# Kernel tuning notes

Measured on AMD Instinct MI355X. Metric: run time of the kernel, lower is better.

## Reference

```python
import jax, jax.numpy as jnp
import numpy as np
from jax import lax

I, H, D1 = 130, 10, 20  # input_size, hidden_size, linear1 width


def _gru_last(x, Wih, Whh, bih, bhh):
    """PyTorch-convention GRU (gate order r,z,n); returns last hidden state [B,H]."""
    # Precompute input projections for all timesteps: [B,T,3H]
    xi = jnp.einsum('bti,gi->btg', x, Wih) + bih
    h0 = jnp.zeros((x.shape[0], H), x.dtype)

    def step(h, xt):  # xt: [B,3H]
        gh = h @ Whh.T + bhh  # [B,3H]
        r = jax.nn.sigmoid(xt[:, :H] + gh[:, :H])
        z = jax.nn.sigmoid(xt[:, H:2 * H] + gh[:, H:2 * H])
        n = jnp.tanh(xt[:, 2 * H:] + r * gh[:, 2 * H:])
        h_new = (1.0 - z) * n + z * h
        return h_new, None

    hT, _ = lax.scan(step, h0, jnp.swapaxes(xi, 0, 1))  # scan over time
    return hT


def setup_inputs() -> dict:
    key = jax.random.key(0)
    ks = jax.random.split(key, 12)
    B, T = 2048, 128
    s_ih = 1.0 / np.sqrt(H)
    inp = {
        'ru': jax.random.normal(ks[0], (B, T, I), jnp.float32),
        'en': jax.random.normal(ks[1], (B, T, I), jnp.float32),
        'ru_Wih': jax.random.uniform(ks[2], (3 * H, I), jnp.float32, -s_ih, s_ih),
        'ru_Whh': jax.random.uniform(ks[3], (3 * H, H), jnp.float32, -s_ih, s_ih),
        'ru_bih': jax.random.uniform(ks[4], (3 * H,), jnp.float32, -s_ih, s_ih),
        'ru_bhh': jax.random.uniform(ks[5], (3 * H,), jnp.float32, -s_ih, s_ih),
        'en_Wih': jax.random.uniform(ks[6], (3 * H, I), jnp.float32, -s_ih, s_ih),
        'en_Whh': jax.random.uniform(ks[7], (3 * H, H), jnp.float32, -s_ih, s_ih),
        'en_bih': jax.random.uniform(ks[8], (3 * H,), jnp.float32, -s_ih, s_ih),
        'en_bhh': jax.random.uniform(ks[9], (3 * H,), jnp.float32, -s_ih, s_ih),
        'W1': jax.random.uniform(ks[10], (D1, 2 * H), jnp.float32, -1 / np.sqrt(2 * H), 1 / np.sqrt(2 * H)),
        'b1': jnp.zeros((D1,), jnp.float32),
        'W2': jax.random.uniform(ks[11], (1, D1), jnp.float32, -1 / np.sqrt(D1), 1 / np.sqrt(D1)),
        'b2': jnp.zeros((1,), jnp.float32),
    }
    return inp


def reference(ru, en, ru_Wih, ru_Whh, ru_bih, ru_bhh,
              en_Wih, en_Whh, en_bih, en_bhh, W1, b1, W2, b2):
    ru_h = _gru_last(ru, ru_Wih, ru_Whh, ru_bih, ru_bhh)  # [B,H] (last timestep output)
    en_h = _gru_last(en, en_Wih, en_Whh, en_bih, en_bhh)  # [B,H]
    grus_out = jnp.concatenate([ru_h, en_h], axis=1)       # [B,2H]
    h1 = grus_out @ W1.T + b1                              # [B,20] (no activation in original)
    out = h1 @ W2.T + b2                                   # [B,1]
    return out
```

## Files before the change

kernel.cpp:

```cpp
#include <hip/hip_runtime.h>


#define BB 2048
#define TT 128
#define II 130

__device__ __forceinline__ float sigmoidf_fast(float x) {
    return __fdividef(1.f, 1.f + __expf(-x));
}
__device__ __forceinline__ float tanhf_fast(float x) {
    float ax = fabsf(x);
    float e = __expf(-2.f * ax);
    float t = __fdividef(1.f - e, 1.f + e);
    return copysignf(t, x);
}

__global__ __launch_bounds__(256, 4)
void gru_fused(const float* __restrict__ ru, const float* __restrict__ en,
               const float* __restrict__ ruWih, const float* __restrict__ ruWhh,
               const float* __restrict__ rubih, const float* __restrict__ rubhh,
               const float* __restrict__ enWih, const float* __restrict__ enWhh,
               const float* __restrict__ enbih, const float* __restrict__ enbhh,
               const float* __restrict__ W1, const float* __restrict__ b1,
               const float* __restrict__ W2, const float* __restrict__ b2,
               float* __restrict__ out)
{
    const int tid  = threadIdx.x;
    const int wv   = tid >> 6;
    const int lane = tid & 63;
    const int g    = lane & 31;
    const int h    = lane >> 5;
    const int wid  = blockIdx.x * 4 + wv;
    const int gru  = wid >> 11;
    const int b    = wid & (BB - 1);

    const float* __restrict__ x   = gru ? en    : ru;
    const float* __restrict__ Wih = gru ? enWih : ruWih;
    const float* __restrict__ Whh = gru ? enWhh : ruWhh;
    const float* __restrict__ bih = gru ? enbih : rubih;
    const float* __restrict__ bhh = gru ? enbhh : rubhh;

    __shared__ __align__(16) float lds[4][176];
    float* __restrict__ X    = lds[wv];
    float* __restrict__ PRE  = X + 132;
    float* __restrict__ Hbuf = X + 164;

    const int gq = (g < 30) ? g : 0;
    float wih[64];
    #pragma unroll
    for (int j = 0; j < 64; ++j) wih[j] = Wih[gq * II + h * 64 + j];
    const float w_e = Wih[gq * II + 128 + h];
    float whh[10];
    #pragma unroll
    for (int k = 0; k < 10; ++k) whh[k] = Whh[gq * 10 + k];
    const float bihg = bih[gq];
    const float bhhg = bhh[gq];

    if (lane < 12) Hbuf[lane] = 0.f;
    float hown = 0.f;

    const float* __restrict__ xrow = x + (size_t)b * (TT * II);

    float xa = xrow[lane];
    float xb = xrow[64 + lane];
    float xc = (lane < 2) ? xrow[128 + lane] : 0.f;

    for (int t = 0; t < TT; ++t) {
        X[lane] = xa;
        X[64 + lane] = xb;
        if (lane < 2) X[128 + lane] = xc;

        {
            const int tn = (t < TT - 1) ? t + 1 : t;
            const float* __restrict__ xn = xrow + (size_t)tn * II;
            xa = xn[lane];
            xb = xn[64 + lane];
            xc = (lane < 2) ? xn[128 + lane] : 0.f;
        }

        const float4 h03 = *(const float4*)(Hbuf);
        const float4 h47 = *(const float4*)(Hbuf + 4);
        const float2 h89 = *(const float2*)(Hbuf + 8);
        float gh0 = fmaf(whh[0], h03.x, bhhg);
        float gh1 = whh[1] * h03.y;
        gh0 = fmaf(whh[2], h03.z, gh0);
        gh1 = fmaf(whh[3], h03.w, gh1);
        gh0 = fmaf(whh[4], h47.x, gh0);
        gh1 = fmaf(whh[5], h47.y, gh1);
        gh0 = fmaf(whh[6], h47.z, gh0);
        gh1 = fmaf(whh[7], h47.w, gh1);
        gh0 = fmaf(whh[8], h89.x, gh0);
        gh1 = fmaf(whh[9], h89.y, gh1);
        const float gh = gh0 + gh1;

        float s0 = 0.f, s1 = 0.f, s2 = 0.f, s3 = 0.f;
        const float4* __restrict__ xb4 = (const float4*)(X + h * 64);
        #pragma unroll
        for (int c = 0; c < 16; ++c) {
            const float4 v = xb4[c];
            s0 = fmaf(wih[4 * c + 0], v.x, s0);
            s1 = fmaf(wih[4 * c + 1], v.y, s1);
            s2 = fmaf(wih[4 * c + 2], v.z, s2);
            s3 = fmaf(wih[4 * c + 3], v.w, s3);
        }
        float s = (s0 + s1) + (s2 + s3);
        s = fmaf(w_e, X[128 + h], s);
        s += __shfl_xor(s, 32);

        const float xi  = s + bihg;
        const float pre = xi + gh;

        if (lane < 30) PRE[lane] = pre;
        const float rpre = PRE[(g - 20) & 31];
        const float zpre = PRE[(g - 10) & 31];

        const float r = sigmoidf_fast(rpre);
        const float z = sigmoidf_fast(zpre);
        const float n = tanhf_fast(xi + r * gh);
        const float hnew = (1.f - z) * n + z * hown;
        hown = hnew;

        if (lane >= 20 && lane < 30) Hbuf[lane - 20] = hnew;
    }

    float val = 0.f;
    if (lane < 10) {
        const float hk = Hbuf[lane];
        float v = 0.f;
        #pragma unroll
        for (int d = 0; d < 20; ++d)
            v = fmaf(W2[d], W1[d * 20 + gru * 10 + lane], v);
        val = v * hk;
        if (lane == 0 && gru == 0) {
            float c = b2[0];
            #pragma unroll
            for (int d = 0; d < 20; ++d) c = fmaf(W2[d], b1[d], c);
            val += c;
        }
    }
    #pragma unroll
    for (int o = 32; o > 0; o >>= 1) val += __shfl_xor(val, o);
    if (lane == 0) atomicAdd(&out[b], val);
}

extern "C" void kernel_launch(void* const* d_in, const int* in_sizes, int n_in,
                              void* d_out, int out_size, void* d_ws, size_t ws_size,
                              hipStream_t stream) {
    (void)in_sizes; (void)n_in; (void)d_ws; (void)ws_size;
    const float* ru    = (const float*)d_in[0];
    const float* en    = (const float*)d_in[1];
    const float* ruWih = (const float*)d_in[2];
    const float* ruWhh = (const float*)d_in[3];
    const float* rubih = (const float*)d_in[4];
    const float* rubhh = (const float*)d_in[5];
    const float* enWih = (const float*)d_in[6];
    const float* enWhh = (const float*)d_in[7];
    const float* enbih = (const float*)d_in[8];
    const float* enbhh = (const float*)d_in[9];
    const float* W1    = (const float*)d_in[10];
    const float* b1    = (const float*)d_in[11];
    const float* W2    = (const float*)d_in[12];
    const float* b2    = (const float*)d_in[13];
    float* out = (float*)d_out;

    hipMemsetAsync(d_out, 0, (size_t)out_size * sizeof(float), stream);
    gru_fused<<<dim3(1024), dim3(256), 0, stream>>>(
        ru, en, ruWih, ruWhh, rubih, rubhh,
        enWih, enWhh, enbih, enbhh, W1, b1, W2, b2, out);
}
```

Before: 143.7 us.

## Split GRU into parallel input-projection GEMM and lightweight recurrent scan kernel

Precomputes input projections for all timesteps into a workspace buffer with a separate fully parallel kernel. A second kernel then runs the recurrence, packing two batch chains per wavefront with per-gate hidden weights in registers. This removes the large input dot product from the serial per-timestep critical path. The cost is extra global memory traffic to write and re-read the projections, and it falls back to the fused kernel if the workspace is too small.

```diff
diff --git a/kernel.cpp b/kernel.cpp
--- a/kernel.cpp
+++ b/kernel.cpp
@@ -4,6 +4,8 @@
 #define BB 2048
 #define TT 128
 #define II 130
+#define ROWS_PER_GRU (BB * TT)
+#define ROWS_TOTAL   (2 * ROWS_PER_GRU)
 
 __device__ __forceinline__ float sigmoidf_fast(float x) {
     return __fdividef(1.f, 1.f + __expf(-x));
@@ -13,6 +15,169 @@
     float e = __expf(-2.f * ax);
     float t = __fdividef(1.f - e, 1.f + e);
     return copysignf(t, x);
+}
+
+__global__ __launch_bounds__(256, 4)
+void xi_gemm(const float* __restrict__ ru, const float* __restrict__ en,
+             const float* __restrict__ ruWih, const float* __restrict__ rubih,
+             const float* __restrict__ enWih, const float* __restrict__ enbih,
+             float* __restrict__ xi)
+{
+    const int tid  = threadIdx.x;
+    const int wv   = tid >> 6;
+    const int lane = tid & 63;
+    const int g    = lane & 31;
+    const int h    = lane >> 5;
+    const int w    = blockIdx.x * 4 + wv;
+    const int gru  = (w >= 4096);
+    const long row0 = (long)w * 64;
+
+    const float* __restrict__ x   = gru ? en    : ru;
+    const float* __restrict__ Wih = gru ? enWih : ruWih;
+    const float* __restrict__ bih = gru ? enbih : rubih;
+
+    const int gq = (g < 30) ? g : 0;
+    float wih[64];
+    #pragma unroll
+    for (int j = 0; j < 64; ++j) wih[j] = Wih[gq * II + h * 64 + j];
+    const float w_e  = Wih[gq * II + 128 + h];
+    const float bihg = bih[gq];
+
+    __shared__ __align__(16) float lds[4][132];
+    float* __restrict__ X = lds[wv];
+
+    const long r0l = row0 - (long)gru * ROWS_PER_GRU;
+    const float* __restrict__ xrow = x + r0l * II;
+    float* __restrict__ xo = xi + row0 * 30;
+
+    float xa = xrow[lane];
+    float xb = xrow[64 + lane];
+    float xc = (lane < 2) ? xrow[128 + lane] : 0.f;
+
+    for (int i = 0; i < 64; ++i) {
+        X[lane] = xa;
+        X[64 + lane] = xb;
+        if (lane < 2) X[128 + lane] = xc;
+
+        {
+            const int inext = (i < 63) ? i + 1 : i;
+            const float* __restrict__ xn = xrow + (long)inext * II;
+            xa = xn[lane];
+            xb = xn[64 + lane];
+            xc = (lane < 2) ? xn[128 + lane] : 0.f;
+        }
+
+        float s0 = 0.f, s1 = 0.f, s2 = 0.f, s3 = 0.f;
+        const float4* __restrict__ xb4 = (const float4*)(X + h * 64);
+        #pragma unroll
+        for (int c = 0; c < 16; ++c) {
+            const float4 v = xb4[c];
+            s0 = fmaf(wih[4 * c + 0], v.x, s0);
+            s1 = fmaf(wih[4 * c + 1], v.y, s1);
+            s2 = fmaf(wih[4 * c + 2], v.z, s2);
+            s3 = fmaf(wih[4 * c + 3], v.w, s3);
+        }
+        float s = (s0 + s1) + (s2 + s3);
+        s = fmaf(w_e, X[128 + h], s);
+        s += __shfl_xor(s, 32);
+
+        if (lane < 30) xo[(long)i * 30 + lane] = s + bihg;
+    }
+}
+
+__global__ __launch_bounds__(256, 4)
+void gru_scan(const float* __restrict__ xi,
+              const float* __restrict__ ruWhh, const float* __restrict__ rubhh,
+              const float* __restrict__ enWhh, const float* __restrict__ enbhh,
+              const float* __restrict__ W1, const float* __restrict__ b1,
+              const float* __restrict__ W2, const float* __restrict__ b2,
+              float* __restrict__ out)
+{
+    const int tid  = threadIdx.x;
+    const int wv   = tid >> 6;
+    const int lane = tid & 63;
+    const int c    = lane >> 5;
+    const int k    = lane & 31;
+    const int kq   = (k < 10) ? k : 0;
+    const int chain = (blockIdx.x * 4 + wv) * 2 + c;
+    const int gru   = chain >> 11;
+    const int b     = chain & (BB - 1);
+
+    const float* __restrict__ Whh = gru ? enWhh : ruWhh;
+    const float* __restrict__ bhh = gru ? enbhh : rubhh;
+
+    float whhR[10], whhZ[10], whhN[10];
+    #pragma unroll
+    for (int j = 0; j < 10; ++j) {
+        whhR[j] = Whh[kq * 10 + j];
+        whhZ[j] = Whh[(10 + kq) * 10 + j];
+        whhN[j] = Whh[(20 + kq) * 10 + j];
+    }
+    const float bR = bhh[kq], bZ = bhh[10 + kq], bN = bhh[20 + kq];
+
+    __shared__ __align__(16) float lds[4][32];
+    float* __restrict__ H = lds[wv] + c * 16;
+    if (k < 12) H[k] = 0.f;
+    float hown = 0.f;
+
+    const float* __restrict__ xrow =
+        xi + ((long)gru * ROWS_PER_GRU + (long)b * TT) * 30;
+
+    float xR0 = xrow[kq],      xZ0 = xrow[10 + kq],  xN0 = xrow[20 + kq];
+    float xR1 = xrow[30 + kq], xZ1 = xrow[40 + kq],  xN1 = xrow[50 + kq];
+
+    for (int t = 0; t < TT; ++t) {
+        const float xR = xR0, xZ = xZ0, xN = xN0;
+        xR0 = xR1; xZ0 = xZ1; xN0 = xN1;
+        {
+            const int tn = (t + 2 < TT) ? t + 2 : TT - 1;
+            const float* __restrict__ xp = xrow + (long)tn * 30;
+            xR1 = xp[kq]; xZ1 = xp[10 + kq]; xN1 = xp[20 + kq];
+        }
+
+        const float4 h03 = *(const float4*)(H);
+        const float4 h47 = *(const float4*)(H + 4);
+        const float2 h89 = *(const float2*)(H + 8);
+
+        float gr = bR, gz = bZ, gn = bN;
+        gr = fmaf(whhR[0], h03.x, gr); gz = fmaf(whhZ[0], h03.x, gz); gn = fmaf(whhN[0], h03.x, gn);
+        gr = fmaf(whhR[1], h03.y, gr); gz = fmaf(whhZ[1], h03.y, gz); gn = fmaf(whhN[1], h03.y, gn);
+        gr = fmaf(whhR[2], h03.z, gr); gz = fmaf(whhZ[2], h03.z, gz); gn = fmaf(whhN[2], h03.z, gn);
+        gr = fmaf(whhR[3], h03.w, gr); gz = fmaf(whhZ[3], h03.w, gz); gn = fmaf(whhN[3], h03.w, gn);
+        gr = fmaf(whhR[4], h47.x, gr); gz = fmaf(whhZ[4], h47.x, gz); gn = fmaf(whhN[4], h47.x, gn);
+        gr = fmaf(whhR[5], h47.y, gr); gz = fmaf(whhZ[5], h47.y, gz); gn = fmaf(whhN[5], h47.y, gn);
+        gr = fmaf(whhR[6], h47.z, gr); gz = fmaf(whhZ[6], h47.z, gz); gn = fmaf(whhN[6], h47.z, gn);
+        gr = fmaf(whhR[7], h47.w, gr); gz = fmaf(whhZ[7], h47.w, gz); gn = fmaf(whhN[7], h47.w, gn);
+        gr = fmaf(whhR[8], h89.x, gr); gz = fmaf(whhZ[8], h89.x, gz); gn = fmaf(whhN[8], h89.x, gn);
+        gr = fmaf(whhR[9], h89.y, gr); gz = fmaf(whhZ[9], h89.y, gz); gn = fmaf(whhN[9], h89.y, gn);
+
+        const float r = sigmoidf_fast(xR + gr);
+        const float z = sigmoidf_fast(xZ + gz);
+        const float n = tanhf_fast(xN + r * gn);
+        const float hnew = fmaf(z, hown - n, n);
+        hown = hnew;
+        if (k < 10) H[k] = hnew;
+    }
+
+    float val = 0.f;
+    if (k < 10) {
+        float v = 0.f;
+        #pragma unroll
+        for (int d = 0; d < 20; ++d)
+            v = fmaf(W2[d], W1[d * 20 + gru * 10 + k], v);
+        val = v * hown;
+        if (k == 0 && gru == 0) {
+            float c0 = b2[0];
+            #pragma unroll
+            for (int d = 0; d < 20; ++d) c0 = fmaf(W2[d], b1[d], c0);
+            val += c0;
+        }
+    }
+    val += __shfl_xor(val, 8);
+    val += __shfl_xor(val, 4);
+    val += __shfl_xor(val, 2);
+    val += __shfl_xor(val, 1);
+    if (k == 0) atomicAdd(&out[b], val);
 }
 
 __global__ __launch_bounds__(256, 4)
@@ -60,7 +225,6 @@
     float hown = 0.f;
 
     const float* __restrict__ xrow = x + (size_t)b * (TT * II);
-
     float xa = xrow[lane];
     float xb = xrow[64 + lane];
     float xc = (lane < 2) ? xrow[128 + lane] : 0.f;
@@ -69,7 +233,6 @@
         X[lane] = xa;
         X[64 + lane] = xb;
         if (lane < 2) X[128 + lane] = xc;
-
         {
             const int tn = (t < TT - 1) ? t + 1 : t;
             const float* __restrict__ xn = xrow + (size_t)tn * II;
@@ -77,7 +240,6 @@
             xb = xn[64 + lane];
             xc = (lane < 2) ? xn[128 + lane] : 0.f;
         }
-
         const float4 h03 = *(const float4*)(Hbuf);
         const float4 h47 = *(const float4*)(Hbuf + 4);
         const float2 h89 = *(const float2*)(Hbuf + 8);
@@ -107,19 +269,16 @@
         s = fmaf(w_e, X[128 + h], s);
         s += __shfl_xor(s, 32);
 
-        const float xi  = s + bihg;
-        const float pre = xi + gh;
-
+        const float xiv = s + bihg;
+        const float pre = xiv + gh;
         if (lane < 30) PRE[lane] = pre;
         const float rpre = PRE[(g - 20) & 31];
         const float zpre = PRE[(g - 10) & 31];
-
         const float r = sigmoidf_fast(rpre);
         const float z = sigmoidf_fast(zpre);
-        const float n = tanhf_fast(xi + r * gh);
+        const float n = tanhf_fast(xiv + r * gh);
         const float hnew = (1.f - z) * n + z * hown;
         hown = hnew;
-
         if (lane >= 20 && lane < 30) Hbuf[lane - 20] = hnew;
     }
 
@@ -132,10 +291,10 @@
             v = fmaf(W2[d], W1[d * 20 + gru * 10 + lane], v);
         val = v * hk;
         if (lane == 0 && gru == 0) {
-            float c = b2[0];
+            float c0 = b2[0];
             #pragma unroll
-            for (int d = 0; d < 20; ++d) c = fmaf(W2[d], b1[d], c);
-            val += c;
+            for (int d = 0; d < 20; ++d) c0 = fmaf(W2[d], b1[d], c0);
+            val += c0;
         }
     }
     #pragma unroll
@@ -146,7 +305,7 @@
 extern "C" void kernel_launch(void* const* d_in, const int* in_sizes, int n_in,
                               void* d_out, int out_size, void* d_ws, size_t ws_size,
                               hipStream_t stream) {
-    (void)in_sizes; (void)n_in; (void)d_ws; (void)ws_size;
+    (void)in_sizes; (void)n_in;
     const float* ru    = (const float*)d_in[0];
     const float* en    = (const float*)d_in[1];
     const float* ruWih = (const float*)d_in[2];
@@ -164,7 +323,17 @@
     float* out = (float*)d_out;
 
     hipMemsetAsync(d_out, 0, (size_t)out_size * sizeof(float), stream);
-    gru_fused<<<dim3(1024), dim3(256), 0, stream>>>(
-        ru, en, ruWih, ruWhh, rubih, rubhh,
-        enWih, enWhh, enbih, enbhh, W1, b1, W2, b2, out);
-}
+
+    const size_t xi_bytes = (size_t)ROWS_TOTAL * 30 * sizeof(float);
+    if (ws_size >= xi_bytes) {
+        float* xi = (float*)d_ws;
+        xi_gemm<<<dim3(2048), dim3(256), 0, stream>>>(
+            ru, en, ruWih, rubih, enWih, enbih, xi);
+        gru_scan<<<dim3(512), dim3(256), 0, stream>>>(
+            xi, ruWhh, rubhh, enWhh, enbhh, W1, b1, W2, b2, out);
+    } else {
+        gru_fused<<<dim3(1024), dim3(256), 0, stream>>>(
+            ru, en, ruWih, ruWhh, rubih, rubhh,
+            enWih, enWhh, enbih, enbhh, W1, b1, W2, b2, out);
+    }
+}
```

Result: slower. 163.9 us (+14.1%).
